# Optimization experiments

Measured on AMD Instinct MI355X. Metric: run time of the kernel, lower is better.

Reference implementation:

```python
import jax, jax.numpy as jnp
import numpy as np

N = 50000
E = 800000
IN_C, HID_C, OUT_C = 512, 128, 256


def setup_inputs() -> dict:
    key = jax.random.key(0)
    k1, k2, k3, k4, k5, k6 = jax.random.split(key, 6)
    x = jax.random.normal(k1, (N, IN_C), dtype=jnp.float32)
    edge_index = jax.random.randint(k2, (2, E), 0, N, dtype=jnp.int64)
    # Linear weights stored torch-style as [out, in]; bias per layer
    w1 = jax.random.normal(k3, (HID_C, IN_C), dtype=jnp.float32) * (1.0 / np.sqrt(IN_C))
    b1 = jax.random.normal(k4, (HID_C,), dtype=jnp.float32) * 0.02
    w2 = jax.random.normal(k5, (OUT_C, HID_C), dtype=jnp.float32) * (1.0 / np.sqrt(HID_C))
    b2 = jax.random.normal(k6, (OUT_C,), dtype=jnp.float32) * 0.02
    return {"x": x, "edge_index": edge_index, "w1": w1, "b1": b1, "w2": w2, "b2": b2}


def gcn_conv(x, edge_index, w, b):
    # x: [N, Cin], w: [Cout, Cin] (torch Linear layout), b: [Cout]
    h = x @ w.T                              # [N, Cout]
    src, dst = edge_index[0], edge_index[1]
    msgs = h[src]                            # gather: [E, Cout]
    agg = jax.ops.segment_sum(msgs, dst, num_segments=h.shape[0])  # scatter_add
    return agg + b


def reference(x, edge_index, w1, b1, w2, b2):
    h = gcn_conv(x, edge_index, w1, b1)
    h = jax.nn.relu(h)
    out = gcn_conv(h, edge_index, w2, b2)
    return out
```

## Files before the change

kernel.cpp:

```cpp
#include <hip/hip_runtime.h>

#define NN 50000
#define EE 800000
#define INC 512
#define HIDC 128
#define OUTC 256
#define CAP 64
#define OV_CAP 65536
#define BUILD_BLOCKS 196
#define GB1 782

typedef __attribute__((ext_vector_type(8))) short bf16x8;
typedef __attribute__((ext_vector_type(4))) float f32x4;

__device__ __forceinline__ short f2bf(float f) {
    unsigned u = __float_as_uint(f);
    unsigned r = u + 0x7fff + ((u >> 16) & 1);
    return (short)(r >> 16);
}
__device__ __forceinline__ float bf2f(short s) {
    return __uint_as_float(((unsigned)(unsigned short)s) << 16);
}

template<bool IN_BF16, bool ADDBIAS, bool OUT_BF16>
__device__ __forceinline__ void gemm_core(
    const void* __restrict__ Av, const float* __restrict__ B,
    const float* __restrict__ bias, void* __restrict__ Cv,
    int M, int Nc, int K, int bx, int by,
    short As[64][72], short Bs[128][72])
{
    int tid = threadIdx.x;
    int lane = tid & 63, wave = tid >> 6;
    int row0 = bx * 64, col0 = by * 128;
    int wm = (wave & 1) * 32, wn = (wave >> 1) * 64;
    int l16 = lane & 15, quad = lane >> 4;

    f32x4 acc[2][4];
#pragma unroll
    for (int i = 0; i < 2; i++)
#pragma unroll
        for (int j = 0; j < 4; j++) acc[i][j] = {0.f, 0.f, 0.f, 0.f};

    for (int k0 = 0; k0 < K; k0 += 64) {
        if (IN_BF16) {
            const short* A = (const short*)Av;
#pragma unroll
            for (int w = 0; w < 2; w++) {
                int f = tid + w * 256;
                int rr = f >> 3, c8 = f & 7;
                int gr = row0 + rr;
                bf16x8 v = {0, 0, 0, 0, 0, 0, 0, 0};
                if (gr < M) v = *(const bf16x8*)&A[(long)gr * K + k0 + c8 * 8];
                *(bf16x8*)&As[rr][c8 * 8] = v;
            }
        } else {
            const float* A = (const float*)Av;
#pragma unroll
            for (int w = 0; w < 4; w++) {
                int f = tid + w * 256;
                int rr = f >> 4, c4 = f & 15;
                int gr = row0 + rr;
                float4 v = make_float4(0.f, 0.f, 0.f, 0.f);
                if (gr < M) v = *(const float4*)&A[(long)gr * K + k0 + c4 * 4];
                short4 s;
                s.x = f2bf(v.x); s.y = f2bf(v.y); s.z = f2bf(v.z); s.w = f2bf(v.w);
                *(short4*)&As[rr][c4 * 4] = s;
            }
        }
#pragma unroll
        for (int w = 0; w < 8; w++) {
            int f = tid + w * 256;
            int rr = f >> 4, c4 = f & 15;
            float4 v = *(const float4*)&B[(long)(col0 + rr) * K + k0 + c4 * 4];
            short4 s;
            s.x = f2bf(v.x); s.y = f2bf(v.y); s.z = f2bf(v.z); s.w = f2bf(v.w);
            *(short4*)&Bs[rr][c4 * 4] = s;
        }
        __syncthreads();

#pragma unroll
        for (int kk = 0; kk < 64; kk += 32) {
            bf16x8 af[2], bfr[4];
#pragma unroll
            for (int i = 0; i < 2; i++)
                af[i] = *(const bf16x8*)&As[wm + i * 16 + l16][kk + quad * 8];
#pragma unroll
            for (int j = 0; j < 4; j++)
                bfr[j] = *(const bf16x8*)&Bs[wn + j * 16 + l16][kk + quad * 8];
#pragma unroll
            for (int i = 0; i < 2; i++)
#pragma unroll
                for (int j = 0; j < 4; j++)
                    acc[i][j] = __builtin_amdgcn_mfma_f32_16x16x32_bf16(
                        af[i], bfr[j], acc[i][j], 0, 0, 0);
        }
        __syncthreads();
    }

#pragma unroll
    for (int i = 0; i < 2; i++) {
#pragma unroll
        for (int rr = 0; rr < 4; rr++) {
            int grow = row0 + wm + i * 16 + quad * 4 + rr;
            if (grow < M) {
#pragma unroll
                for (int j = 0; j < 4; j++) {
                    int gcol = col0 + wn + j * 16 + l16;
                    float v = acc[i][j][rr];
                    if (ADDBIAS) v += bias[gcol];
                    if (OUT_BF16)
                        ((short*)Cv)[(long)grow * Nc + gcol] = f2bf(v);
                    else
                        ((float*)Cv)[(long)grow * Nc + gcol] = v;
                }
            }
        }
    }
}

__global__ __launch_bounds__(256) void fat_build_gemm1(
    const int* __restrict__ ei, int* __restrict__ cnt,
    unsigned short* __restrict__ bucket, int* __restrict__ ovcnt,
    int* __restrict__ ovlist,
    const float* __restrict__ x, const float* __restrict__ w1,
    short* __restrict__ h)
{
    __shared__ short As[64][72];
    __shared__ short Bs[128][72];

    if (blockIdx.x < BUILD_BLOCKS) {
        int t = threadIdx.x;
        long base = ((long)blockIdx.x * 256 + t) * 16;
        if (base + 16 <= EE) {
            int4 sv[4], dv[4];
#pragma unroll
            for (int q = 0; q < 4; q++) {
                sv[q] = *(const int4*)&ei[base + q * 4];
                dv[q] = *(const int4*)&ei[EE + base + q * 4];
            }
            const int* sp = (const int*)sv;
            const int* dp = (const int*)dv;
#pragma unroll
            for (int k = 0; k < 16; k++) {
                int src = sp[k], dst = dp[k];
                int pos = atomicAdd(&cnt[dst], 1);
                if (pos < CAP) bucket[(long)dst * CAP + pos] = (unsigned short)src;
                else {
                    int o = atomicAdd(ovcnt, 1);
                    if (o < OV_CAP) { ovlist[o * 2] = src; ovlist[o * 2 + 1] = dst; }
                }
            }
        } else {
            for (int k = 0; k < 16; k++) {
                long e = base + k;
                if (e < EE) {
                    int src = ei[e], dst = ei[EE + e];
                    int pos = atomicAdd(&cnt[dst], 1);
                    if (pos < CAP) bucket[(long)dst * CAP + pos] = (unsigned short)src;
                    else {
                        int o = atomicAdd(ovcnt, 1);
                        if (o < OV_CAP) { ovlist[o * 2] = src; ovlist[o * 2 + 1] = dst; }
                    }
                }
            }
        }
    } else {
        gemm_core<false, false, true>(x, w1, nullptr, h, NN, HIDC, INC,
                                      blockIdx.x - BUILD_BLOCKS, 0, As, Bs);
    }
}

__global__ __launch_bounds__(256) void gemm2_k(
    const short* __restrict__ r2, const float* __restrict__ w2,
    const float* __restrict__ b2, float* __restrict__ out)
{
    __shared__ short As[64][72];
    __shared__ short Bs[128][72];
    gemm_core<true, true, false>(r2, w2, b2, out, NN, OUTC, HIDC,
                                 blockIdx.x, blockIdx.y, As, Bs);
}

template<bool RELU>
__global__ __launch_bounds__(256) void gather_k(
    const short* __restrict__ hsrc, const unsigned short* __restrict__ bucket,
    const int* __restrict__ cnt, const float* __restrict__ bias,
    short* __restrict__ rout)
{
    int t = threadIdx.x;
    int node = blockIdx.x * 16 + (t >> 4);
    int c8 = t & 15;
    if (node >= NN) return;
    int m = cnt[node]; if (m > CAP) m = CAP;
    const unsigned short* bk = bucket + (long)node * CAP;
    float acc[8];
#pragma unroll
    for (int k = 0; k < 8; k++) acc[k] = 0.f;
    int j = 0;
    for (; j + 8 <= m; j += 8) {
        int s[8];
#pragma unroll
        for (int q = 0; q < 8; q++) s[q] = bk[j + q];
        bf16x8 v[8];
#pragma unroll
        for (int q = 0; q < 8; q++)
            v[q] = *(const bf16x8*)&hsrc[((long)s[q] << 7) + c8 * 8];
#pragma unroll
        for (int q = 0; q < 8; q++)
#pragma unroll
            for (int k = 0; k < 8; k++) acc[k] += bf2f(v[q][k]);
    }
    for (; j < m; j++) {
        int s0 = bk[j];
        bf16x8 v0 = *(const bf16x8*)&hsrc[((long)s0 << 7) + c8 * 8];
#pragma unroll
        for (int k = 0; k < 8; k++) acc[k] += bf2f(v0[k]);
    }
    bf16x8 o;
    if (RELU) {
#pragma unroll
        for (int k = 0; k < 8; k++)
            o[k] = f2bf(fmaxf(acc[k] + bias[c8 * 8 + k], 0.f));
    } else {
#pragma unroll
        for (int k = 0; k < 8; k++) o[k] = f2bf(acc[k]);
    }
    *(bf16x8*)&rout[((long)node << 7) + c8 * 8] = o;
}

__global__ __launch_bounds__(128) void ovfix1_k(
    const short* __restrict__ h, const float* __restrict__ b1,
    const unsigned short* __restrict__ bucket, const int* __restrict__ cnt,
    const int* __restrict__ ovcnt, const int* __restrict__ ovlist,
    short* __restrict__ r)
{
    int n = *ovcnt; if (n > OV_CAP) n = OV_CAP;
    int c = threadIdx.x;
    for (int i = 0; i < n; i++) {
        int dst = ovlist[i * 2 + 1];
        bool dup = false;
        for (int i2 = 0; i2 < i; i2++)
            if (ovlist[i2 * 2 + 1] == dst) { dup = true; break; }
        if (dup) continue;
        int m = cnt[dst]; if (m > CAP) m = CAP;
        const unsigned short* bk = bucket + (long)dst * CAP;
        float acc = 0.f;
        for (int j = 0; j < m; j++)
            acc += bf2f(h[(long)bk[j] * 128 + c]);
        for (int i2 = 0; i2 < n; i2++)
            if (ovlist[i2 * 2 + 1] == dst)
                acc += bf2f(h[(long)ovlist[i2 * 2] * 128 + c]);
        r[(long)dst * 128 + c] = f2bf(fmaxf(acc + b1[c], 0.f));
    }
}

__global__ __launch_bounds__(128) void ovfix2_k(
    const short* __restrict__ r, const unsigned short* __restrict__ bucket,
    const int* __restrict__ cnt, const int* __restrict__ ovcnt,
    const int* __restrict__ ovlist, short* __restrict__ r2)
{
    int n = *ovcnt; if (n > OV_CAP) n = OV_CAP;
    int c = threadIdx.x;
    for (int i = 0; i < n; i++) {
        int dst = ovlist[i * 2 + 1];
        bool dup = false;
        for (int i2 = 0; i2 < i; i2++)
            if (ovlist[i2 * 2 + 1] == dst) { dup = true; break; }
        if (dup) continue;
        int m = cnt[dst]; if (m > CAP) m = CAP;
        const unsigned short* bk = bucket + (long)dst * CAP;
        float acc = 0.f;
        for (int j = 0; j < m; j++)
            acc += bf2f(r[(long)bk[j] * 128 + c]);
        for (int i2 = 0; i2 < n; i2++)
            if (ovlist[i2 * 2 + 1] == dst)
                acc += bf2f(r[(long)ovlist[i2 * 2] * 128 + c]);
        r2[(long)dst * 128 + c] = f2bf(acc);
    }
}

extern "C" void kernel_launch(void* const* d_in, const int* in_sizes, int n_in,
                              void* d_out, int out_size, void* d_ws, size_t ws_size,
                              hipStream_t stream) {
    const float* x  = (const float*)d_in[0];
    const int*   ei = (const int*)d_in[1];
    const float* w1 = (const float*)d_in[2];
    const float* b1 = (const float*)d_in[3];
    const float* w2 = (const float*)d_in[4];
    const float* b2 = (const float*)d_in[5];
    float* out = (float*)d_out;

    char* ws = (char*)d_ws;
    size_t off = 0;
    short* h    = (short*)(ws + off); off += (size_t)NN * HIDC * 2;
    short* r    = (short*)(ws + off); off += (size_t)NN * HIDC * 2;
    short* r2   = (short*)(ws + off); off += (size_t)NN * HIDC * 2;
    unsigned short* bucket = (unsigned short*)(ws + off);
    off += (size_t)NN * CAP * 2;
    int* cnt    = (int*)(ws + off);   off += (size_t)NN * 4;
    int* ovcnt  = (int*)(ws + off);   off += 256;
    int* ovlist = (int*)(ws + off);   off += (size_t)OV_CAP * 2 * 4;

    hipMemsetAsync(cnt, 0, (size_t)NN * 4 + 4, stream);

    dim3 blk(256);

    fat_build_gemm1<<<dim3(BUILD_BLOCKS + GB1), blk, 0, stream>>>(
        ei, cnt, bucket, ovcnt, ovlist, x, w1, h);

    gather_k<true><<<dim3(3125), blk, 0, stream>>>(h, bucket, cnt, b1, r);
    ovfix1_k<<<dim3(1), dim3(128), 0, stream>>>(h, b1, bucket, cnt, ovcnt, ovlist, r);

    gather_k<false><<<dim3(3125), blk, 0, stream>>>(r, bucket, cnt, nullptr, r2);
    ovfix2_k<<<dim3(1), dim3(128), 0, stream>>>(r, bucket, cnt, ovcnt, ovlist, r2);

    gemm2_k<<<dim3(GB1, 2), blk, 0, stream>>>(r2, w2, b2, out);
}
```

Baseline: 306.7 us.

## Fuse second gather into GEMM2 and inline overflow handling into gathers

The second neighbor aggregation now writes its 64-row tile straight into shared memory, and the GEMM2 MFMA runs on it in the same kernel, so the intermediate r2 buffer never goes through global memory. The single-block overflow fixup kernels are removed. Overflow edges are now added inside the gather for nodes whose count exceeds the bucket capacity, by scanning the overflow list. This cuts two serial launches and one round trip to global memory. In exchange, the fused kernel has fewer blocks with a long gather phase before its GEMM, and the overflow scan is linear per overflowing node.

```diff
diff --git a/kernel.cpp b/kernel.cpp
--- a/kernel.cpp
+++ b/kernel.cpp
@@ -22,16 +22,14 @@
     return __uint_as_float(((unsigned)(unsigned short)s) << 16);
 }
 
-template<bool IN_BF16, bool ADDBIAS, bool OUT_BF16>
-__device__ __forceinline__ void gemm_core(
-    const void* __restrict__ Av, const float* __restrict__ B,
-    const float* __restrict__ bias, void* __restrict__ Cv,
-    int M, int Nc, int K, int bx, int by,
+__device__ __forceinline__ void gemm1_core(
+    const float* __restrict__ A, const float* __restrict__ B,
+    short* __restrict__ C, int bx,
     short As[64][72], short Bs[128][72])
 {
     int tid = threadIdx.x;
     int lane = tid & 63, wave = tid >> 6;
-    int row0 = bx * 64, col0 = by * 128;
+    int row0 = bx * 64;
     int wm = (wave & 1) * 32, wn = (wave >> 1) * 64;
     int l16 = lane & 15, quad = lane >> 4;
 
@@ -41,37 +39,23 @@
 #pragma unroll
         for (int j = 0; j < 4; j++) acc[i][j] = {0.f, 0.f, 0.f, 0.f};
 
-    for (int k0 = 0; k0 < K; k0 += 64) {
-        if (IN_BF16) {
-            const short* A = (const short*)Av;
-#pragma unroll
-            for (int w = 0; w < 2; w++) {
-                int f = tid + w * 256;
-                int rr = f >> 3, c8 = f & 7;
-                int gr = row0 + rr;
-                bf16x8 v = {0, 0, 0, 0, 0, 0, 0, 0};
-                if (gr < M) v = *(const bf16x8*)&A[(long)gr * K + k0 + c8 * 8];
-                *(bf16x8*)&As[rr][c8 * 8] = v;
-            }
-        } else {
-            const float* A = (const float*)Av;
-#pragma unroll
-            for (int w = 0; w < 4; w++) {
-                int f = tid + w * 256;
-                int rr = f >> 4, c4 = f & 15;
-                int gr = row0 + rr;
-                float4 v = make_float4(0.f, 0.f, 0.f, 0.f);
-                if (gr < M) v = *(const float4*)&A[(long)gr * K + k0 + c4 * 4];
-                short4 s;
-                s.x = f2bf(v.x); s.y = f2bf(v.y); s.z = f2bf(v.z); s.w = f2bf(v.w);
-                *(short4*)&As[rr][c4 * 4] = s;
-            }
+    for (int k0 = 0; k0 < INC; k0 += 64) {
+#pragma unroll
+        for (int w = 0; w < 4; w++) {
+            int f = tid + w * 256;
+            int rr = f >> 4, c4 = f & 15;
+            int gr = row0 + rr;
+            float4 v = make_float4(0.f, 0.f, 0.f, 0.f);
+            if (gr < NN) v = *(const float4*)&A[(long)gr * INC + k0 + c4 * 4];
+            short4 s;
+            s.x = f2bf(v.x); s.y = f2bf(v.y); s.z = f2bf(v.z); s.w = f2bf(v.w);
+            *(short4*)&As[rr][c4 * 4] = s;
         }
 #pragma unroll
         for (int w = 0; w < 8; w++) {
             int f = tid + w * 256;
             int rr = f >> 4, c4 = f & 15;
-            float4 v = *(const float4*)&B[(long)(col0 + rr) * K + k0 + c4 * 4];
+            float4 v = *(const float4*)&B[(long)rr * INC + k0 + c4 * 4];
             short4 s;
             s.x = f2bf(v.x); s.y = f2bf(v.y); s.z = f2bf(v.z); s.w = f2bf(v.w);
             *(short4*)&Bs[rr][c4 * 4] = s;
@@ -98,24 +82,15 @@
     }
 
 #pragma unroll
-    for (int i = 0; i < 2; i++) {
+    for (int i = 0; i < 2; i++)
 #pragma unroll
         for (int rr = 0; rr < 4; rr++) {
             int grow = row0 + wm + i * 16 + quad * 4 + rr;
-            if (grow < M) {
-#pragma unroll
-                for (int j = 0; j < 4; j++) {
-                    int gcol = col0 + wn + j * 16 + l16;
-                    float v = acc[i][j][rr];
-                    if (ADDBIAS) v += bias[gcol];
-                    if (OUT_BF16)
-                        ((short*)Cv)[(long)grow * Nc + gcol] = f2bf(v);
-                    else
-                        ((float*)Cv)[(long)grow * Nc + gcol] = v;
-                }
-            }
-        }
-    }
+            if (grow < NN)
+#pragma unroll
+                for (int j = 0; j < 4; j++)
+                    C[(long)grow * HIDC + wn + j * 16 + l16] = f2bf(acc[i][j][rr]);
+        }
 }
 
 __global__ __launch_bounds__(256) void fat_build_gemm1(
@@ -165,116 +140,154 @@
             }
         }
     } else {
-        gemm_core<false, false, true>(x, w1, nullptr, h, NN, HIDC, INC,
-                                      blockIdx.x - BUILD_BLOCKS, 0, As, Bs);
-    }
-}
-
-__global__ __launch_bounds__(256) void gemm2_k(
-    const short* __restrict__ r2, const float* __restrict__ w2,
-    const float* __restrict__ b2, float* __restrict__ out)
-{
-    __shared__ short As[64][72];
-    __shared__ short Bs[128][72];
-    gemm_core<true, true, false>(r2, w2, b2, out, NN, OUTC, HIDC,
-                                 blockIdx.x, blockIdx.y, As, Bs);
-}
-
-template<bool RELU>
-__global__ __launch_bounds__(256) void gather_k(
-    const short* __restrict__ hsrc, const unsigned short* __restrict__ bucket,
-    const int* __restrict__ cnt, const float* __restrict__ bias,
-    short* __restrict__ rout)
+        gemm1_core(x, w1, h, blockIdx.x - BUILD_BLOCKS, As, Bs);
+    }
+}
+
+__device__ __forceinline__ void gather_row(
+    const short* __restrict__ hsrc, const unsigned short* __restrict__ bk,
+    int m0, const int* __restrict__ ovcnt, const int* __restrict__ ovlist,
+    int node, int c8, float acc[8])
+{
+#pragma unroll
+    for (int k = 0; k < 8; k++) acc[k] = 0.f;
+    int m = m0 > CAP ? CAP : m0;
+    int j = 0;
+    for (; j + 8 <= m; j += 8) {
+        int s[8];
+#pragma unroll
+        for (int q = 0; q < 8; q++) s[q] = bk[j + q];
+        bf16x8 v[8];
+#pragma unroll
+        for (int q = 0; q < 8; q++)
+            v[q] = *(const bf16x8*)&hsrc[((long)s[q] << 7) + c8 * 8];
+#pragma unroll
+        for (int q = 0; q < 8; q++)
+#pragma unroll
+            for (int k = 0; k < 8; k++) acc[k] += bf2f(v[q][k]);
+    }
+    for (; j < m; j++) {
+        int s0 = bk[j];
+        bf16x8 v0 = *(const bf16x8*)&hsrc[((long)s0 << 7) + c8 * 8];
+#pragma unroll
+        for (int k = 0; k < 8; k++) acc[k] += bf2f(v0[k]);
+    }
+    if (m0 > CAP) {
+        int n = *ovcnt; if (n > OV_CAP) n = OV_CAP;
+        for (int i = 0; i < n; i++) {
+            if (ovlist[i * 2 + 1] == node) {
+                bf16x8 v0 = *(const bf16x8*)&hsrc[((long)ovlist[i * 2] << 7) + c8 * 8];
+#pragma unroll
+                for (int k = 0; k < 8; k++) acc[k] += bf2f(v0[k]);
+            }
+        }
+    }
+}
+
+__global__ __launch_bounds__(256) void gather1_k(
+    const short* __restrict__ h, const unsigned short* __restrict__ bucket,
+    const int* __restrict__ cnt, const int* __restrict__ ovcnt,
+    const int* __restrict__ ovlist, const float* __restrict__ b1,
+    short* __restrict__ r)
 {
     int t = threadIdx.x;
     int node = blockIdx.x * 16 + (t >> 4);
     int c8 = t & 15;
     if (node >= NN) return;
-    int m = cnt[node]; if (m > CAP) m = CAP;
-    const unsigned short* bk = bucket + (long)node * CAP;
     float acc[8];
-#pragma unroll
-    for (int k = 0; k < 8; k++) acc[k] = 0.f;
-    int j = 0;
-    for (; j + 8 <= m; j += 8) {
-        int s[8];
-#pragma unroll
-        for (int q = 0; q < 8; q++) s[q] = bk[j + q];
-        bf16x8 v[8];
-#pragma unroll
-        for (int q = 0; q < 8; q++)
-            v[q] = *(const bf16x8*)&hsrc[((long)s[q] << 7) + c8 * 8];
-#pragma unroll
-        for (int q = 0; q < 8; q++)
-#pragma unroll
-            for (int k = 0; k < 8; k++) acc[k] += bf2f(v[q][k]);
-    }
-    for (; j < m; j++) {
-        int s0 = bk[j];
-        bf16x8 v0 = *(const bf16x8*)&hsrc[((long)s0 << 7) + c8 * 8];
-#pragma unroll
-        for (int k = 0; k < 8; k++) acc[k] += bf2f(v0[k]);
-    }
+    gather_row(h, bucket + (long)node * CAP, cnt[node], ovcnt, ovlist,
+               node, c8, acc);
     bf16x8 o;
-    if (RELU) {
-#pragma unroll
-        for (int k = 0; k < 8; k++)
-            o[k] = f2bf(fmaxf(acc[k] + bias[c8 * 8 + k], 0.f));
-    } else {
-#pragma unroll
-        for (int k = 0; k < 8; k++) o[k] = f2bf(acc[k]);
-    }
-    *(bf16x8*)&rout[((long)node << 7) + c8 * 8] = o;
-}
-
-__global__ __launch_bounds__(128) void ovfix1_k(
-    const short* __restrict__ h, const float* __restrict__ b1,
-    const unsigned short* __restrict__ bucket, const int* __restrict__ cnt,
-    const int* __restrict__ ovcnt, const int* __restrict__ ovlist,
-    short* __restrict__ r)
-{
-    int n = *ovcnt; if (n > OV_CAP) n = OV_CAP;
-    int c = threadIdx.x;
-    for (int i = 0; i < n; i++) {
-        int dst = ovlist[i * 2 + 1];
-        bool dup = false;
-        for (int i2 = 0; i2 < i; i2++)
-            if (ovlist[i2 * 2 + 1] == dst) { dup = true; break; }
-        if (dup) continue;
-        int m = cnt[dst]; if (m > CAP) m = CAP;
-        const unsigned short* bk = bucket + (long)dst * CAP;
-        float acc = 0.f;
-        for (int j = 0; j < m; j++)
-            acc += bf2f(h[(long)bk[j] * 128 + c]);
-        for (int i2 = 0; i2 < n; i2++)
-            if (ovlist[i2 * 2 + 1] == dst)
-                acc += bf2f(h[(long)ovlist[i2 * 2] * 128 + c]);
-        r[(long)dst * 128 + c] = f2bf(fmaxf(acc + b1[c], 0.f));
-    }
-}
-
-__global__ __launch_bounds__(128) void ovfix2_k(
+#pragma unroll
+    for (int k = 0; k < 8; k++)
+        o[k] = f2bf(fmaxf(acc[k] + b1[c8 * 8 + k], 0.f));
+    *(bf16x8*)&r[((long)node << 7) + c8 * 8] = o;
+}
+
+__global__ __launch_bounds__(256) void fused_gather2_gemm2(
     const short* __restrict__ r, const unsigned short* __restrict__ bucket,
     const int* __restrict__ cnt, const int* __restrict__ ovcnt,
-    const int* __restrict__ ovlist, short* __restrict__ r2)
-{
-    int n = *ovcnt; if (n > OV_CAP) n = OV_CAP;
-    int c = threadIdx.x;
-    for (int i = 0; i < n; i++) {
-        int dst = ovlist[i * 2 + 1];
-        bool dup = false;
-        for (int i2 = 0; i2 < i; i2++)
-            if (ovlist[i2 * 2 + 1] == dst) { dup = true; break; }
-        if (dup) continue;
-        int m = cnt[dst]; if (m > CAP) m = CAP;
-        const unsigned short* bk = bucket + (long)dst * CAP;
-        float acc = 0.f;
-        for (int j = 0; j < m; j++)
-            acc += bf2f(r[(long)bk[j] * 128 + c]);
-        for (int i2 = 0; i2 < n; i2++)
-            if (ovlist[i2 * 2 + 1] == dst)
-                acc += bf2f(r[(long)ovlist[i2 * 2] * 128 + c]);
-        r2[(long)dst * 128 + c] = f2bf(acc);
+    const int* __restrict__ ovlist,
+    const float* __restrict__ w2, const float* __restrict__ b2,
+    float* __restrict__ out)
+{
+    __shared__ short As[64][136];
+    __shared__ short Bs[128][136];
+
+    int t = threadIdx.x;
+    int lane = t & 63, wave = t >> 6;
+    int grp = t >> 4, c8 = t & 15;
+    int l16 = lane & 15, quad = lane >> 4;
+    int row0 = blockIdx.x * 64;
+
+    for (int it = 0; it < 4; it++) {
+        int rr = grp * 4 + it;
+        int node = row0 + rr;
+        float acc[8];
+        if (node < NN) {
+            gather_row(r, bucket + (long)node * CAP, cnt[node], ovcnt, ovlist,
+                       node, c8, acc);
+        } else {
+#pragma unroll
+            for (int k = 0; k < 8; k++) acc[k] = 0.f;
+        }
+        bf16x8 o;
+#pragma unroll
+        for (int k = 0; k < 8; k++) o[k] = f2bf(acc[k]);
+        *(bf16x8*)&As[rr][c8 * 8] = o;
+    }
+    __syncthreads();
+
+    int wm = (wave & 1) * 32, wn = (wave >> 1) * 64;
+#pragma unroll
+    for (int by = 0; by < 2; by++) {
+#pragma unroll
+        for (int w = 0; w < 16; w++) {
+            int f = t + w * 256;
+            int rr = f >> 5, c4 = f & 31;
+            float4 v = *(const float4*)&w2[(long)(by * 128 + rr) * HIDC + c4 * 4];
+            short4 s;
+            s.x = f2bf(v.x); s.y = f2bf(v.y); s.z = f2bf(v.z); s.w = f2bf(v.w);
+            *(short4*)&Bs[rr][c4 * 4] = s;
+        }
+        __syncthreads();
+
+        f32x4 acc[2][4];
+#pragma unroll
+        for (int i = 0; i < 2; i++)
+#pragma unroll
+            for (int j = 0; j < 4; j++) acc[i][j] = {0.f, 0.f, 0.f, 0.f};
+
+#pragma unroll
+        for (int kk = 0; kk < 128; kk += 32) {
+            bf16x8 af[2], bfr[4];
+#pragma unroll
+            for (int i = 0; i < 2; i++)
+                af[i] = *(const bf16x8*)&As[wm + i * 16 + l16][kk + quad * 8];
+#pragma unroll
+            for (int j = 0; j < 4; j++)
+                bfr[j] = *(const bf16x8*)&Bs[wn + j * 16 + l16][kk + quad * 8];
+#pragma unroll
+            for (int i = 0; i < 2; i++)
+#pragma unroll
+                for (int j = 0; j < 4; j++)
+                    acc[i][j] = __builtin_amdgcn_mfma_f32_16x16x32_bf16(
+                        af[i], bfr[j], acc[i][j], 0, 0, 0);
+        }
+
+#pragma unroll
+        for (int i = 0; i < 2; i++)
+#pragma unroll
+            for (int rr = 0; rr < 4; rr++) {
+                int grow = row0 + wm + i * 16 + quad * 4 + rr;
+                if (grow < NN)
+#pragma unroll
+                    for (int j = 0; j < 4; j++) {
+                        int gcol = by * 128 + wn + j * 16 + l16;
+                        out[(long)grow * OUTC + gcol] = acc[i][j][rr] + b2[gcol];
+                    }
+            }
+        __syncthreads();
     }
 }
 
@@ -293,7 +306,6 @@
     size_t off = 0;
     short* h    = (short*)(ws + off); off += (size_t)NN * HIDC * 2;
     short* r    = (short*)(ws + off); off += (size_t)NN * HIDC * 2;
-    short* r2   = (short*)(ws + off); off += (size_t)NN * HIDC * 2;
     unsigned short* bucket = (unsigned short*)(ws + off);
     off += (size_t)NN * CAP * 2;
     int* cnt    = (int*)(ws + off);   off += (size_t)NN * 4;
@@ -307,11 +319,8 @@
     fat_build_gemm1<<<dim3(BUILD_BLOCKS + GB1), blk, 0, stream>>>(
         ei, cnt, bucket, ovcnt, ovlist, x, w1, h);
 
-    gather_k<true><<<dim3(3125), blk, 0, stream>>>(h, bucket, cnt, b1, r);
-    ovfix1_k<<<dim3(1), dim3(128), 0, stream>>>(h, b1, bucket, cnt, ovcnt, ovlist, r);
-
-    gather_k<false><<<dim3(3125), blk, 0, stream>>>(r, bucket, cnt, nullptr, r2);
-    ovfix2_k<<<dim3(1), dim3(128), 0, stream>>>(r, bucket, cnt, ovcnt, ovlist, r2);
-
-    gemm2_k<<<dim3(GB1, 2), blk, 0, stream>>>(r2, w2, b2, out);
-}
+    gather1_k<<<dim3(3125), blk, 0, stream>>>(h, bucket, cnt, ovcnt, ovlist, b1, r);
+
+    fused_gather2_gemm2<<<dim3(GB1), blk, 0, stream>>>(
+        r, bucket, cnt, ovcnt, ovlist, w2, b2, out);
+}
```

Measured after the change: 305.2 us. Within noise of the previous version (-0.5%).
